# Optimization experiments

Measured on AMD Instinct MI355X. Metric: run time of the kernel, lower is better.

The kernel has to match this reference:

```python
import jax, jax.numpy as jnp
import numpy as np

LN_EPS = 1e-5
ATTN_EPS = 1e-6
NHEAD = 8

def layer_norm(x, g, b):
    m = jnp.mean(x, axis=-1, keepdims=True)
    v = jnp.var(x, axis=-1, keepdims=True)
    return (x - m) * jax.lax.rsqrt(v + LN_EPS) * g + b

def rope_maps(H, W, D):
    # 2D RoPE over the head dim: even freq-pairs encode row position i, odd pairs col position j.
    quarter = D // 4
    div = jnp.exp(jnp.arange(quarter, dtype=jnp.float32) * (-np.log(10000.0) / quarter))
    ang_i = jnp.arange(1, H + 1, dtype=jnp.float32)[:, None, None] * div  # [H,1,q]
    ang_j = jnp.arange(1, W + 1, dtype=jnp.float32)[None, :, None] * div  # [1,W,q]
    ang_i = jnp.broadcast_to(ang_i, (H, W, quarter))
    ang_j = jnp.broadcast_to(ang_j, (H, W, quarter))
    sin_h = jnp.stack((jnp.sin(ang_i), jnp.sin(ang_j)), axis=-1).reshape(H, W, D // 2)
    cos_h = jnp.stack((jnp.cos(ang_i), jnp.cos(ang_j)), axis=-1).reshape(H, W, D // 2)
    # repeat_interleave(2) to act on (x_{2i}, x_{2i+1}) rotation pairs
    return jnp.repeat(sin_h, 2, axis=-1), jnp.repeat(cos_h, 2, axis=-1)  # each [H,W,D]

def rotate_half(x):
    xp = x.reshape(*x.shape[:-1], -1, 2)
    x1, x2 = xp[..., 0], xp[..., 1]
    return jnp.stack((-x2, x1), axis=-1).reshape(x.shape)

def apply_rope(x, sin, cos, H, W):
    # x: [N, L, nh, D] with L = H*W
    N, L, nh, D = x.shape
    xg = x.reshape(N, H, W, nh, D)
    s = sin[None, :, :, None, :]
    c = cos[None, :, :, None, :]
    out = xg * c + rotate_half(xg) * s
    return out.reshape(N, L, nh, D)

def rope_linear_attention(q, k, v, H, W):
    # elu+1 feature map linear attention (LoFTR) with 2D RoPE on Q/K
    Q = jax.nn.elu(q) + 1.0
    K = jax.nn.elu(k) + 1.0
    v_len = v.shape[1]
    v = v / v_len  # prevent overflow, restored at the end
    sin, cos = rope_maps(H, W, Q.shape[-1])
    Q = apply_rope(Q, sin, cos, H, W)
    K = apply_rope(K, sin, cos, H, W)
    KV = jnp.einsum('nshd,nshv->nhdv', K, v)                       # [N,nh,D,D]
    Z = 1.0 / (jnp.einsum('nlhd,nhd->nlh', Q, K.sum(axis=1)) + ATTN_EPS)
    return jnp.einsum('nlhd,nhdv,nlh->nlhv', Q, KV, Z) * v_len     # [N,L,nh,D]

def setup_inputs() -> dict:
    key = jax.random.key(0)
    ks = jax.random.split(key, 8)
    N, L, C = 4, 16384, 256
    s = 0.02
    return {
        'x': jax.random.normal(ks[0], (N, L, C), jnp.float32),
        'source': jax.random.normal(ks[1], (N, L, C), jnp.float32),
        'Wq': jax.random.normal(ks[2], (C, C), jnp.float32) * s,
        'Wk': jax.random.normal(ks[3], (C, C), jnp.float32) * s,
        'Wv': jax.random.normal(ks[4], (C, C), jnp.float32) * s,
        'Wm': jax.random.normal(ks[5], (C, C), jnp.float32) * s,
        'W1': jax.random.normal(ks[6], (2 * C, 2 * C), jnp.float32) * s,
        'W2': jax.random.normal(ks[7], (C, 2 * C), jnp.float32) * s,
        'ln1_g': jnp.ones((C,), jnp.float32),
        'ln1_b': jnp.zeros((C,), jnp.float32),
        'ln2_g': jnp.ones((C,), jnp.float32),
        'ln2_b': jnp.zeros((C,), jnp.float32),
        'H': 128,
        'W': 128,
    }

def reference(x, source, Wq, Wk, Wv, Wm, W1, W2, ln1_g, ln1_b, ln2_g, ln2_b, H, W):
    N, L, C = x.shape
    D = C // NHEAD
    q = (x @ Wq.T).reshape(N, L, NHEAD, D)
    k = (source @ Wk.T).reshape(N, L, NHEAD, D)
    v = (source @ Wv.T).reshape(N, L, NHEAD, D)
    msg = rope_linear_attention(q, k, v, H, W).reshape(N, L, C)
    msg = layer_norm(msg @ Wm.T, ln1_g, ln1_b)
    h = jnp.concatenate([x, msg], axis=-1)              # [N,L,2C]
    h = jax.nn.relu(h @ W1.T) @ W2.T                    # [N,L,C]
    msg = layer_norm(h, ln2_g, ln2_b)
    return x + msg
```

## Files before the change

### kernel.cpp

```cpp
#include <hip/hip_runtime.h>
#include <hip/hip_bf16.h>
#include <math.h>

#define NB 4
#define LL 16384
#define CC 256
#define NHD 8
#define DH 32
#define MROWS (NB*LL)

typedef __hip_bfloat16 bf16;
typedef __attribute__((ext_vector_type(8))) short short8;
typedef __attribute__((ext_vector_type(4))) float floatx4;

__device__ __forceinline__ float u2f(unsigned short u) {
  return __uint_as_float(((unsigned)u) << 16);
}
__device__ __forceinline__ unsigned short f2u(float f) {
  bf16 t = __float2bfloat16(f);
  unsigned short u;
  __builtin_memcpy(&u, &t, 2);
  return u;
}

__global__ __launch_bounds__(256) void convert_kernel(
    const float* __restrict__ in, bf16* __restrict__ out, int n8)
{
  int i = blockIdx.x*256 + threadIdx.x;
  if (i >= n8) return;
  const float4* p = (const float4*)in + (size_t)i*2;
  float4 f0 = p[0], f1 = p[1];
  unsigned short t[8] = {f2u(f0.x),f2u(f0.y),f2u(f0.z),f2u(f0.w),
                         f2u(f1.x),f2u(f1.y),f2u(f1.z),f2u(f1.w)};
  *(uint4*)(out + (size_t)i*8) = *(uint4*)t;
}

__global__ __launch_bounds__(256) void convert_weights_kernel(
    const float* __restrict__ Wq, const float* __restrict__ Wk,
    const float* __restrict__ Wv, const float* __restrict__ Wm,
    const float* __restrict__ W1, const float* __restrict__ W2,
    bf16* __restrict__ dst)
{
  int i = blockIdx.x*256 + threadIdx.x;
  const float* src; int off8;
  if      (i < 8192)  { src = Wq; off8 = i; }
  else if (i < 16384) { src = Wk; off8 = i-8192; }
  else if (i < 24576) { src = Wv; off8 = i-16384; }
  else if (i < 32768) { src = Wm; off8 = i-24576; }
  else if (i < 65536) { src = W1; off8 = i-32768; }
  else                { src = W2; off8 = i-65536; }
  const float4* p = (const float4*)src + (size_t)off8*2;
  float4 f0 = p[0], f1 = p[1];
  unsigned short t[8] = {f2u(f0.x),f2u(f0.y),f2u(f0.z),f2u(f0.w),
                         f2u(f1.x),f2u(f1.y),f2u(f1.z),f2u(f1.w)};
  *(uint4*)(dst + (size_t)i*8) = *(uint4*)t;
}

template<int EPI>
__global__ __launch_bounds__(64, 4) void gemm_w64(
    const bf16* __restrict__ A0, int K0, const bf16* __restrict__ A1,
    const bf16* __restrict__ B, bf16* __restrict__ C,
    int M, int N, int K)
{
  __shared__ __align__(16) unsigned short As[64*32];
  __shared__ __align__(16) unsigned short Bs[64*32];
  const int lane = threadIdx.x;
  const int l15 = lane & 15, quad = lane >> 4;

  const int nbn = N >> 6;
  const int lg  = (nbn == 4) ? 2 : 3;
  const int id  = blockIdx.x;
  const int xcd = id & 7;
  const int seq = id >> 3;
  const int bn  = seq & (nbn - 1);
  const int bm  = ((seq >> lg) << 3) + xcd;

  const int srow  = lane >> 2;
  const int skcol = (lane & 3) << 3;

  floatx4 acc[4][4] = {};

  for (int kt = 0; kt < K; kt += 32) {
    const bf16* aSrc; int lda, kof;
    if (kt < K0) { aSrc = A0; lda = K0;     kof = kt; }
    else         { aSrc = A1; lda = K - K0; kof = kt - K0; }
    #pragma unroll
    for (int c = 0; c < 4; c++) {
      const bf16* gp = aSrc + (size_t)(bm*64 + c*16 + srow)*lda + kof + skcol;
      __builtin_amdgcn_global_load_lds(
          (const __attribute__((address_space(1))) void*)gp,
          (__attribute__((address_space(3))) void*)(As + c*512 + lane*8),
          16, 0, 0);
    }
    #pragma unroll
    for (int c = 0; c < 4; c++) {
      const bf16* gp = B + (size_t)(bn*64 + c*16 + srow)*K + kt + skcol;
      __builtin_amdgcn_global_load_lds(
          (const __attribute__((address_space(1))) void*)gp,
          (__attribute__((address_space(3))) void*)(Bs + c*512 + lane*8),
          16, 0, 0);
    }
    asm volatile("s_waitcnt vmcnt(0)" ::: "memory");
    __builtin_amdgcn_sched_barrier(0);
    short8 a[4], b[4];
    #pragma unroll
    for (int i = 0; i < 4; i++) {
      a[i] = *(const short8*)&As[(i*16 + l15)*32 + quad*8];
      b[i] = *(const short8*)&Bs[(i*16 + l15)*32 + quad*8];
    }
    #pragma unroll
    for (int i = 0; i < 4; i++)
      #pragma unroll
      for (int j = 0; j < 4; j++)
        acc[i][j] = __builtin_amdgcn_mfma_f32_16x16x32_bf16(a[i], b[j], acc[i][j], 0, 0, 0);
    __builtin_amdgcn_sched_barrier(0);
  }

  const int row0 = bm*64 + quad*4;
  const int col0 = bn*64 + l15;
  if (EPI == 2) {
    const int pp_e = l15 >> 1;
    const int pp_o = pp_e + 8;
    const int par  = pp_e & 1;
    const float dv_e = __expf(-1.15129254650564f * (float)(pp_e >> 1));
    const float dv_o = __expf(-1.15129254650564f * (float)(pp_o >> 1));
    const float sgn = (l15 & 1) ? 1.f : -1.f;
    #pragma unroll
    for (int i = 0; i < 4; i++) {
      #pragma unroll
      for (int r = 0; r < 4; r++) {
        int row = row0 + i*16 + r;
        int l = row & (LL-1);
        float pos = par ? (float)((l & 127) + 1) : (float)((l >> 7) + 1);
        float ae = pos * dv_e, ao = pos * dv_o;
        float se = __sinf(ae), ce = __cosf(ae);
        float so = __sinf(ao), co = __cosf(ao);
        #pragma unroll
        for (int j = 0; j < 4; j++) {
          float s = (j & 1) ? so : se;
          float c = (j & 1) ? co : ce;
          float v = acc[i][j][r];
          v = v > 0.f ? v + 1.f : __expf(v);
          float p = __shfl_xor(v, 1, 64);
          float o = fmaf(v, c, sgn * p * s);
          C[(size_t)row*N + (col0 + j*16)] = __float2bfloat16(o);
        }
      }
    }
  } else {
    #pragma unroll
    for (int i = 0; i < 4; i++)
      #pragma unroll
      for (int j = 0; j < 4; j++)
        #pragma unroll
        for (int r = 0; r < 4; r++) {
          float v = acc[i][j][r];
          if (EPI == 1) v = fmaxf(v, 0.f);
          C[(size_t)(row0 + i*16 + r)*N + (col0 + j*16)] = __float2bfloat16(v);
        }
  }
}

#define KVPAD 36
__global__ __launch_bounds__(256) void kv_kernel(
    const bf16* __restrict__ Kr, const bf16* __restrict__ V,
    float* __restrict__ KVp, float* __restrict__ Ksp)
{
  __shared__ __align__(16) float Kf[128*KVPAD];
  __shared__ __align__(16) float Vf[128*KVPAD];
  const int nh = blockIdx.x;
  const int n = nh >> 3, h = nh & 7;
  const int cs = blockIdx.y;
  const int s0 = cs << 9;
  const int tid = threadIdx.x;
  const int d = tid >> 3, e0 = (tid & 7) << 2;

  float acc0 = 0.f, acc1 = 0.f, acc2 = 0.f, acc3 = 0.f, ks = 0.f;

  for (int sub = 0; sub < 4; sub++) {
    const int sb = s0 + sub*128;
    #pragma unroll
    for (int u = tid; u < 512; u += 256) {
      int row = u >> 2, d0 = (u & 3) << 3;
      size_t g = (((size_t)(n*LL + sb + row)*NHD + h) << 5) + d0;
      short8 k8 = *(const short8*)(Kr + g);
      short8 v8 = *(const short8*)(V + g);
      float* kp = &Kf[row*KVPAD + d0];
      float* vp = &Vf[row*KVPAD + d0];
      float4 ka = {u2f((unsigned short)k8[0]), u2f((unsigned short)k8[1]),
                   u2f((unsigned short)k8[2]), u2f((unsigned short)k8[3])};
      float4 kb = {u2f((unsigned short)k8[4]), u2f((unsigned short)k8[5]),
                   u2f((unsigned short)k8[6]), u2f((unsigned short)k8[7])};
      float4 va = {u2f((unsigned short)v8[0]), u2f((unsigned short)v8[1]),
                   u2f((unsigned short)v8[2]), u2f((unsigned short)v8[3])};
      float4 vb = {u2f((unsigned short)v8[4]), u2f((unsigned short)v8[5]),
                   u2f((unsigned short)v8[6]), u2f((unsigned short)v8[7])};
      *(float4*)kp = ka; *(float4*)(kp+4) = kb;
      *(float4*)vp = va; *(float4*)(vp+4) = vb;
    }
    __syncthreads();
    #pragma unroll 8
    for (int ss = 0; ss < 128; ss++) {
      float kd = Kf[ss*KVPAD + d];
      float4 v4 = *(const float4*)&Vf[ss*KVPAD + e0];
      acc0 = fmaf(kd, v4.x, acc0);
      acc1 = fmaf(kd, v4.y, acc1);
      acc2 = fmaf(kd, v4.z, acc2);
      acc3 = fmaf(kd, v4.w, acc3);
      ks += kd;
    }
    __syncthreads();
  }

  float* kvp = KVp + (((size_t)nh << 5) + cs) * 1024 + (tid << 2);
  kvp[0] = acc0; kvp[1] = acc1; kvp[2] = acc2; kvp[3] = acc3;
  if ((tid & 7) == 0) Ksp[(((size_t)nh << 5) + cs) * 32 + d] = ks;
}

__global__ __launch_bounds__(256) void reduce_kv_kernel(
    const float* __restrict__ KVp, const float* __restrict__ Ksp,
    float* __restrict__ KV, float* __restrict__ Ksum)
{
  const int nh = blockIdx.x;
  const int tid = threadIdx.x;
  float4 acc = {0.f,0.f,0.f,0.f};
  #pragma unroll 8
  for (int cs = 0; cs < 32; cs++) {
    float4 p = *(const float4*)(KVp + (((size_t)nh << 5) + cs) * 1024 + (tid << 2));
    acc.x += p.x; acc.y += p.y; acc.z += p.z; acc.w += p.w;
  }
  *(float4*)(KV + ((size_t)nh << 10) + (tid << 2)) = acc;
  if (tid < 32) {
    float s = 0.f;
    #pragma unroll 8
    for (int cs = 0; cs < 32; cs++)
      s += Ksp[(((size_t)nh << 5) + cs) * 32 + tid];
    Ksum[(nh << 5) + tid] = s;
  }
}

__global__ __launch_bounds__(256) void attn_out_kernel(
    const bf16* __restrict__ Qr, const float* __restrict__ KV,
    const float* __restrict__ Ksum, bf16* __restrict__ Out)
{
  __shared__ float KVs[8192];
  __shared__ float Kss[256];
  __shared__ float Qs[16][256];
  const int blk = blockIdx.x;
  const int n = blk >> 10;
  const int tid = threadIdx.x;
  const size_t rowBase = (size_t)blk * 16;
  for (int i = tid; i < 8192; i += 256) KVs[i] = KV[((size_t)n << 13) + i];
  Kss[tid] = Ksum[(n << 8) + tid];
  #pragma unroll
  for (int it = 0; it < 2; it++) {
    int i = it*256 + tid;
    short8 u = *(const short8*)(Qr + (rowBase << 8) + (size_t)i*8);
    float* qp = ((float*)Qs) + (size_t)i*8;
    #pragma unroll
    for (int j = 0; j < 8; j++) qp[j] = u2f((unsigned short)u[j]);
  }
  __syncthreads();
  const int h = tid >> 5, e = tid & 31;
  const float* kvh = &KVs[(h << 10) + e];
  const float* ksh = &Kss[h << 5];
  for (int r = 0; r < 16; r++) {
    const float* qh = &Qs[r][h << 5];
    float denom = 1e-6f;
    float num = 0.f;
    #pragma unroll
    for (int d = 0; d < 32; d++) {
      float qd = qh[d];
      denom = fmaf(qd, ksh[d], denom);
      num   = fmaf(qd, kvh[d << 5], num);
    }
    Out[((rowBase + r) << 8) + tid] = __float2bfloat16(num / denom);
  }
}

__global__ __launch_bounds__(256) void ln_kernel(
    const bf16* __restrict__ X, const float* __restrict__ g, const float* __restrict__ b,
    bf16* __restrict__ Out)
{
  __shared__ float ps[4], psq[4], stat[2];
  int row = blockIdx.x, tid = threadIdx.x;
  float v = __bfloat162float(X[((size_t)row << 8) + tid]);
  float s = v, sq = v*v;
  #pragma unroll
  for (int o = 32; o > 0; o >>= 1) {
    s  += __shfl_down(s, o, 64);
    sq += __shfl_down(sq, o, 64);
  }
  if ((tid & 63) == 0) { ps[tid>>6] = s; psq[tid>>6] = sq; }
  __syncthreads();
  if (tid == 0) {
    float S = ps[0]+ps[1]+ps[2]+ps[3];
    float SQ = psq[0]+psq[1]+psq[2]+psq[3];
    float mean = S * (1.f/256.f);
    float var = SQ * (1.f/256.f) - mean*mean;
    stat[0] = mean; stat[1] = rsqrtf(var + 1e-5f);
  }
  __syncthreads();
  float mean = stat[0], rstd = stat[1];
  Out[((size_t)row << 8) + tid] = __float2bfloat16(
      (v - mean)*rstd*g[tid] + b[tid]);
}

__global__ __launch_bounds__(256) void ln_add_kernel(
    const bf16* __restrict__ X, const float* __restrict__ g, const float* __restrict__ b,
    const float* __restrict__ xin, float* __restrict__ Out)
{
  __shared__ float ps[4], psq[4], stat[2];
  int row = blockIdx.x, tid = threadIdx.x;
  size_t idx = ((size_t)row << 8) + tid;
  float v = __bfloat162float(X[idx]);
  float s = v, sq = v*v;
  #pragma unroll
  for (int o = 32; o > 0; o >>= 1) {
    s  += __shfl_down(s, o, 64);
    sq += __shfl_down(sq, o, 64);
  }
  if ((tid & 63) == 0) { ps[tid>>6] = s; psq[tid>>6] = sq; }
  __syncthreads();
  if (tid == 0) {
    float S = ps[0]+ps[1]+ps[2]+ps[3];
    float SQ = psq[0]+psq[1]+psq[2]+psq[3];
    float mean = S * (1.f/256.f);
    float var = SQ * (1.f/256.f) - mean*mean;
    stat[0] = mean; stat[1] = rsqrtf(var + 1e-5f);
  }
  __syncthreads();
  float mean = stat[0], rstd = stat[1];
  float lnv = (v - mean)*rstd*g[tid] + b[tid];
  Out[idx] = xin[idx] + lnv;
}

extern "C" void kernel_launch(void* const* d_in, const int* in_sizes, int n_in,
                              void* d_out, int out_size, void* d_ws, size_t ws_size,
                              hipStream_t stream) {
  const float* x   = (const float*)d_in[0];
  const float* src = (const float*)d_in[1];
  const float* Wq  = (const float*)d_in[2];
  const float* Wk  = (const float*)d_in[3];
  const float* Wv  = (const float*)d_in[4];
  const float* Wm  = (const float*)d_in[5];
  const float* W1  = (const float*)d_in[6];
  const float* W2  = (const float*)d_in[7];
  const float* g1  = (const float*)d_in[8];
  const float* b1  = (const float*)d_in[9];
  const float* g2  = (const float*)d_in[10];
  const float* b2  = (const float*)d_in[11];
  float* out = (float*)d_out;

  bf16* ws = (bf16*)d_ws;
  const size_t BUFH = (size_t)MROWS * CC;
  bf16* R0 = ws;
  bf16* R1 = ws + BUFH;
  bf16* R2 = ws + 2*BUFH;
  bf16* R3 = ws + 3*BUFH;
  bf16* WB = ws + 4*BUFH;
  bf16* wq = WB, *wk = WB+65536, *wv = WB+131072, *wm = WB+196608,
      *w1 = WB+262144, *w2 = WB+524288;
  float* KV   = (float*)(WB + 655360);
  float* Ksum = KV + NB*NHD*DH*DH;
  float* KVp = out;
  float* Ksp = out + 32*32*1024;

  dim3 blk(256);
  dim3 blk64(64);
  const int n8 = MROWS*CC/8;
  convert_kernel<<<(n8+255)/256, blk, 0, stream>>>(x,   R0, n8);
  convert_kernel<<<(n8+255)/256, blk, 0, stream>>>(src, R1, n8);
  convert_weights_kernel<<<320, blk, 0, stream>>>(Wq, Wk, Wv, Wm, W1, W2, WB);

  const int G256 = (MROWS/64)*(CC/64);
  const int G512 = (MROWS/64)*(2*CC/64);
  gemm_w64<2><<<G256, blk64, 0, stream>>>(R1, CC, nullptr, wk, R2, MROWS, CC, CC);
  gemm_w64<0><<<G256, blk64, 0, stream>>>(R1, CC, nullptr, wv, R3, MROWS, CC, CC);
  kv_kernel<<<dim3(NB*NHD, 32), blk, 0, stream>>>(R2, R3, KVp, Ksp);
  reduce_kv_kernel<<<NB*NHD, blk, 0, stream>>>(KVp, Ksp, KV, Ksum);
  gemm_w64<2><<<G256, blk64, 0, stream>>>(R0, CC, nullptr, wq, R1, MROWS, CC, CC);
  attn_out_kernel<<<MROWS/16, blk, 0, stream>>>(R1, KV, Ksum, R2);
  gemm_w64<0><<<G256, blk64, 0, stream>>>(R2, CC, nullptr, wm, R3, MROWS, CC, CC);
  ln_kernel<<<MROWS, blk, 0, stream>>>(R3, g1, b1, R3);
  gemm_w64<1><<<G512, blk64, 0, stream>>>(R0, CC, R3, w1, R1, MROWS, 2*CC, 2*CC);
  gemm_w64<0><<<G256, blk64, 0, stream>>>(nullptr, 0, R1, w2, R3, MROWS, CC, 2*CC);
  ln_add_kernel<<<MROWS, blk, 0, stream>>>(R3, g2, b2, x, out);
}
```

Measured before the change: 555.8 us.

## Double-buffer GEMM LDS tiles and stage output through LDS for vector stores

The single-wave GEMM now double-buffers its A/B tiles in one shared LDS array, issuing the next k-tile's global-to-LDS loads before computing the current one and waiting only for the older batch. Each lane now loads one full row segment, with the LDS layout changed to match. The epilogue writes results into LDS first, then performs coalesced 16-byte row stores instead of scattered 2-byte stores. This adds LDS usage (16KB per block), which may reduce occupancy, and it depends on the vmcnt counts being exactly right.

```diff
diff --git a/kernel.cpp b/kernel.cpp
--- a/kernel.cpp
+++ b/kernel.cpp
@@ -62,8 +62,7 @@
     const bf16* __restrict__ B, bf16* __restrict__ C,
     int M, int N, int K)
 {
-  __shared__ __align__(16) unsigned short As[64*32];
-  __shared__ __align__(16) unsigned short Bs[64*32];
+  __shared__ __align__(16) unsigned short SM[8192];
   const int lane = threadIdx.x;
   const int l15 = lane & 15, quad = lane >> 4;
 
@@ -75,38 +74,50 @@
   const int bn  = seq & (nbn - 1);
   const int bm  = ((seq >> lg) << 3) + xcd;
 
-  const int srow  = lane >> 2;
-  const int skcol = (lane & 3) << 3;
+  const bf16* bRow = B + (size_t)(bn*64 + lane)*K;
 
   floatx4 acc[4][4] = {};
-
-  for (int kt = 0; kt < K; kt += 32) {
-    const bf16* aSrc; int lda, kof;
-    if (kt < K0) { aSrc = A0; lda = K0;     kof = kt; }
-    else         { aSrc = A1; lda = K - K0; kof = kt - K0; }
-    #pragma unroll
-    for (int c = 0; c < 4; c++) {
-      const bf16* gp = aSrc + (size_t)(bm*64 + c*16 + srow)*lda + kof + skcol;
-      __builtin_amdgcn_global_load_lds(
-          (const __attribute__((address_space(1))) void*)gp,
-          (__attribute__((address_space(3))) void*)(As + c*512 + lane*8),
-          16, 0, 0);
-    }
-    #pragma unroll
-    for (int c = 0; c < 4; c++) {
-      const bf16* gp = B + (size_t)(bn*64 + c*16 + srow)*K + kt + skcol;
-      __builtin_amdgcn_global_load_lds(
-          (const __attribute__((address_space(1))) void*)gp,
-          (__attribute__((address_space(3))) void*)(Bs + c*512 + lane*8),
-          16, 0, 0);
-    }
-    asm volatile("s_waitcnt vmcnt(0)" ::: "memory");
+  const int NT = K >> 5;
+
+  #define STAGE(t, buf)                                                     \
+  {                                                                         \
+    int kt_ = (t) << 5;                                                     \
+    const bf16* aSrc_; int lda_, kof_;                                      \
+    if (kt_ < K0) { aSrc_ = A0; lda_ = K0;     kof_ = kt_; }                \
+    else          { aSrc_ = A1; lda_ = K - K0; kof_ = kt_ - K0; }           \
+    const bf16* aRow_ = aSrc_ + (size_t)(bm*64 + lane)*lda_ + kof_;         \
+    _Pragma("unroll")                                                       \
+    for (int c = 0; c < 4; c++) {                                           \
+      __builtin_amdgcn_global_load_lds(                                     \
+          (const __attribute__((address_space(1))) void*)(aRow_ + c*8),     \
+          (__attribute__((address_space(3))) void*)(SM + ((buf)<<11) + c*512 + lane*8), \
+          16, 0, 0);                                                        \
+    }                                                                       \
+    const bf16* bRk_ = bRow + kt_;                                          \
+    _Pragma("unroll")                                                       \
+    for (int c = 0; c < 4; c++) {                                           \
+      __builtin_amdgcn_global_load_lds(                                     \
+          (const __attribute__((address_space(1))) void*)(bRk_ + c*8),      \
+          (__attribute__((address_space(3))) void*)(SM + 4096 + ((buf)<<11) + c*512 + lane*8), \
+          16, 0, 0);                                                        \
+    }                                                                       \
+  }
+
+  STAGE(0, 0);
+  for (int t = 0; t < NT; ++t) {
+    const int cur = t & 1;
+    if (t + 1 < NT) {
+      STAGE(t + 1, cur ^ 1);
+      asm volatile("s_waitcnt vmcnt(8)" ::: "memory");
+    } else {
+      asm volatile("s_waitcnt vmcnt(0)" ::: "memory");
+    }
     __builtin_amdgcn_sched_barrier(0);
     short8 a[4], b[4];
     #pragma unroll
     for (int i = 0; i < 4; i++) {
-      a[i] = *(const short8*)&As[(i*16 + l15)*32 + quad*8];
-      b[i] = *(const short8*)&Bs[(i*16 + l15)*32 + quad*8];
+      a[i] = *(const short8*)&SM[(cur<<11) + quad*512 + (i*16 + l15)*8];
+      b[i] = *(const short8*)&SM[4096 + (cur<<11) + quad*512 + (i*16 + l15)*8];
     }
     #pragma unroll
     for (int i = 0; i < 4; i++)
@@ -115,9 +126,10 @@
         acc[i][j] = __builtin_amdgcn_mfma_f32_16x16x32_bf16(a[i], b[j], acc[i][j], 0, 0, 0);
     __builtin_amdgcn_sched_barrier(0);
   }
-
-  const int row0 = bm*64 + quad*4;
-  const int col0 = bn*64 + l15;
+  #undef STAGE
+
+  #define CSTR 88
+  unsigned short* Cs = SM;
   if (EPI == 2) {
     const int pp_e = l15 >> 1;
     const int pp_o = pp_e + 8;
@@ -129,7 +141,8 @@
     for (int i = 0; i < 4; i++) {
       #pragma unroll
       for (int r = 0; r < 4; r++) {
-        int row = row0 + i*16 + r;
+        int rloc = i*16 + quad*4 + r;
+        int row  = bm*64 + rloc;
         int l = row & (LL-1);
         float pos = par ? (float)((l & 127) + 1) : (float)((l >> 7) + 1);
         float ae = pos * dv_e, ao = pos * dv_o;
@@ -143,7 +156,7 @@
           v = v > 0.f ? v + 1.f : __expf(v);
           float p = __shfl_xor(v, 1, 64);
           float o = fmaf(v, c, sgn * p * s);
-          C[(size_t)row*N + (col0 + j*16)] = __float2bfloat16(o);
+          Cs[rloc*CSTR + j*16 + l15] = f2u(o);
         }
       }
     }
@@ -156,9 +169,20 @@
         for (int r = 0; r < 4; r++) {
           float v = acc[i][j][r];
           if (EPI == 1) v = fmaxf(v, 0.f);
-          C[(size_t)(row0 + i*16 + r)*N + (col0 + j*16)] = __float2bfloat16(v);
+          Cs[(i*16 + quad*4 + r)*CSTR + j*16 + l15] = f2u(v);
         }
   }
+  asm volatile("s_waitcnt lgkmcnt(0)" ::: "memory");
+  __builtin_amdgcn_sched_barrier(0);
+  const size_t cb = (size_t)(bm*64)*N + bn*64;
+  #pragma unroll
+  for (int s = 0; s < 8; s++) {
+    int unit = s*64 + lane;
+    int row = unit >> 3, c8 = unit & 7;
+    short8 vv = *(const short8*)&Cs[row*CSTR + c8*8];
+    *(short8*)(C + cb + (size_t)row*N + c8*8) = vv;
+  }
+  #undef CSTR
 }
 
 #define KVPAD 36
```

Result: slower. 757.2 us (+36.2%).

## Use 128x128 four-wave GEMM tiles with swizzled LDS and fused K/V projection

Applied to the files above, without the earlier changes.

Replaces the single-wave 64x64 GEMM with a 256-thread 128x128 tile kernel. The A tile is staged in XOR-swizzled LDS and shared by two waves along N, while B fragments are read directly from global memory into registers. The K and V projections are fused into one GEMM over the concatenated weight rows, with RoPE applied only to the K half. This aims to raise arithmetic intensity and cut launches and A re-reads, at the cost of a block-wide barrier per k-step and uncached global B loads.

```diff
diff --git a/kernel.cpp b/kernel.cpp
--- a/kernel.cpp
+++ b/kernel.cpp
@@ -57,26 +57,26 @@
 }
 
 template<int EPI>
-__global__ __launch_bounds__(64, 4) void gemm_w64(
+__global__ __launch_bounds__(256) void gemm_m97(
     const bf16* __restrict__ A0, int K0, const bf16* __restrict__ A1,
-    const bf16* __restrict__ B, bf16* __restrict__ C,
+    const bf16* __restrict__ B, bf16* __restrict__ C, bf16* __restrict__ C2,
     int M, int N, int K)
 {
-  __shared__ __align__(16) unsigned short As[64*32];
-  __shared__ __align__(16) unsigned short Bs[64*32];
-  const int lane = threadIdx.x;
+  __shared__ __align__(16) unsigned short As[4096];
+  const int tid  = threadIdx.x;
+  const int lane = tid & 63, wave = tid >> 6;
+  const int wm = wave & 1, wn = wave >> 1;
   const int l15 = lane & 15, quad = lane >> 4;
 
-  const int nbn = N >> 6;
-  const int lg  = (nbn == 4) ? 2 : 3;
-  const int id  = blockIdx.x;
-  const int xcd = id & 7;
-  const int seq = id >> 3;
-  const int bn  = seq & (nbn - 1);
-  const int bm  = ((seq >> lg) << 3) + xcd;
-
-  const int srow  = lane >> 2;
-  const int skcol = (lane & 3) << 3;
+  const int nbn = N >> 7;
+  const int sh  = (nbn == 2) ? 4 : 5;
+  const int w   = blockIdx.x & ((1 << sh) - 1);
+  const int g   = blockIdx.x >> sh;
+  const int bm  = g*8 + (w & 7);
+  const int bn  = w >> 3;
+
+  const bf16* bBase = B + (size_t)(bn*128 + wn*64 + l15)*K;
+  const int swz = quad ^ ((l15 >> 1) & 3);
 
   floatx4 acc[4][4] = {};
 
@@ -85,40 +85,37 @@
     if (kt < K0) { aSrc = A0; lda = K0;     kof = kt; }
     else         { aSrc = A1; lda = K - K0; kof = kt - K0; }
     #pragma unroll
-    for (int c = 0; c < 4; c++) {
-      const bf16* gp = aSrc + (size_t)(bm*64 + c*16 + srow)*lda + kof + skcol;
+    for (int m = 0; m < 2; m++) {
+      int U = m*256 + tid;
+      int row = U >> 2, q = U & 3;
+      int gq = q ^ ((row >> 1) & 3);
+      const bf16* gp = aSrc + (size_t)(bm*128 + row)*lda + kof + gq*8;
       __builtin_amdgcn_global_load_lds(
           (const __attribute__((address_space(1))) void*)gp,
-          (__attribute__((address_space(3))) void*)(As + c*512 + lane*8),
+          (__attribute__((address_space(3))) void*)(As + (size_t)U*8),
           16, 0, 0);
     }
-    #pragma unroll
-    for (int c = 0; c < 4; c++) {
-      const bf16* gp = B + (size_t)(bn*64 + c*16 + srow)*K + kt + skcol;
-      __builtin_amdgcn_global_load_lds(
-          (const __attribute__((address_space(1))) void*)gp,
-          (__attribute__((address_space(3))) void*)(Bs + c*512 + lane*8),
-          16, 0, 0);
-    }
-    asm volatile("s_waitcnt vmcnt(0)" ::: "memory");
-    __builtin_amdgcn_sched_barrier(0);
-    short8 a[4], b[4];
-    #pragma unroll
-    for (int i = 0; i < 4; i++) {
-      a[i] = *(const short8*)&As[(i*16 + l15)*32 + quad*8];
-      b[i] = *(const short8*)&Bs[(i*16 + l15)*32 + quad*8];
-    }
+    short8 b[4];
+    #pragma unroll
+    for (int j = 0; j < 4; j++)
+      b[j] = *(const short8*)(bBase + (size_t)(j*16)*K + kt + quad*8);
+    __syncthreads();
+    short8 a[4];
+    #pragma unroll
+    for (int i = 0; i < 4; i++)
+      a[i] = *(const short8*)&As[((wm*64 + i*16 + l15)*4 + swz)*8];
     #pragma unroll
     for (int i = 0; i < 4; i++)
       #pragma unroll
       for (int j = 0; j < 4; j++)
         acc[i][j] = __builtin_amdgcn_mfma_f32_16x16x32_bf16(a[i], b[j], acc[i][j], 0, 0, 0);
-    __builtin_amdgcn_sched_barrier(0);
-  }
-
-  const int row0 = bm*64 + quad*4;
-  const int col0 = bn*64 + l15;
-  if (EPI == 2) {
+    __syncthreads();
+  }
+
+  const int row0 = bm*128 + wm*64 + quad*4;
+  const int col0 = bn*128 + wn*64 + l15;
+  const bool doRope = (EPI == 2) || (EPI == 3 && bn < 2);
+  if (doRope) {
     const int pp_e = l15 >> 1;
     const int pp_o = pp_e + 8;
     const int par  = pp_e & 1;
@@ -143,10 +140,20 @@
           v = v > 0.f ? v + 1.f : __expf(v);
           float p = __shfl_xor(v, 1, 64);
           float o = fmaf(v, c, sgn * p * s);
-          C[(size_t)row*N + (col0 + j*16)] = __float2bfloat16(o);
+          int stride = (EPI == 3) ? 256 : N;
+          C[(size_t)row*stride + (col0 + j*16)] = __float2bfloat16(o);
         }
       }
     }
+  } else if (EPI == 3) {
+    #pragma unroll
+    for (int i = 0; i < 4; i++)
+      #pragma unroll
+      for (int j = 0; j < 4; j++)
+        #pragma unroll
+        for (int r = 0; r < 4; r++)
+          C2[(size_t)(row0 + i*16 + r)*256 + (col0 - 256 + j*16)] =
+              __float2bfloat16(acc[i][j][r]);
   } else {
     #pragma unroll
     for (int i = 0; i < 4; i++)
@@ -367,23 +374,21 @@
   float* Ksp = out + 32*32*1024;
 
   dim3 blk(256);
-  dim3 blk64(64);
   const int n8 = MROWS*CC/8;
   convert_kernel<<<(n8+255)/256, blk, 0, stream>>>(x,   R0, n8);
   convert_kernel<<<(n8+255)/256, blk, 0, stream>>>(src, R1, n8);
   convert_weights_kernel<<<320, blk, 0, stream>>>(Wq, Wk, Wv, Wm, W1, W2, WB);
 
-  const int G256 = (MROWS/64)*(CC/64);
-  const int G512 = (MROWS/64)*(2*CC/64);
-  gemm_w64<2><<<G256, blk64, 0, stream>>>(R1, CC, nullptr, wk, R2, MROWS, CC, CC);
-  gemm_w64<0><<<G256, blk64, 0, stream>>>(R1, CC, nullptr, wv, R3, MROWS, CC, CC);
+  const int G256 = (MROWS/128)*(CC/128);
+  const int G512 = (MROWS/128)*(2*CC/128);
+  gemm_m97<3><<<G512, blk, 0, stream>>>(R1, CC, nullptr, wk, R2, R3, MROWS, 2*CC, CC);
   kv_kernel<<<dim3(NB*NHD, 32), blk, 0, stream>>>(R2, R3, KVp, Ksp);
   reduce_kv_kernel<<<NB*NHD, blk, 0, stream>>>(KVp, Ksp, KV, Ksum);
-  gemm_w64<2><<<G256, blk64, 0, stream>>>(R0, CC, nullptr, wq, R1, MROWS, CC, CC);
+  gemm_m97<2><<<G256, blk, 0, stream>>>(R0, CC, nullptr, wq, R1, nullptr, MROWS, CC, CC);
   attn_out_kernel<<<MROWS/16, blk, 0, stream>>>(R1, KV, Ksum, R2);
-  gemm_w64<0><<<G256, blk64, 0, stream>>>(R2, CC, nullptr, wm, R3, MROWS, CC, CC);
+  gemm_m97<0><<<G256, blk, 0, stream>>>(R2, CC, nullptr, wm, R3, nullptr, MROWS, CC, CC);
   ln_kernel<<<MROWS, blk, 0, stream>>>(R3, g1, b1, R3);
-  gemm_w64<1><<<G512, blk64, 0, stream>>>(R0, CC, R3, w1, R1, MROWS, 2*CC, 2*CC);
-  gemm_w64<0><<<G256, blk64, 0, stream>>>(nullptr, 0, R1, w2, R3, MROWS, CC, 2*CC);
+  gemm_m97<1><<<G512, blk, 0, stream>>>(R0, CC, R3, w1, R1, nullptr, MROWS, 2*CC, 2*CC);
+  gemm_m97<0><<<G256, blk, 0, stream>>>(nullptr, 0, R1, w2, R3, nullptr, MROWS, CC, 2*CC);
   ln_add_kernel<<<MROWS, blk, 0, stream>>>(R3, g2, b2, x, out);
 }
```

Result: slower. 612.0 us (+10.1%).
